# Kernel tuning notes

Hardware: AMD Instinct MI355X
Metric: run time of the kernel (lower is better)

## Reference

```python
import jax, jax.numpy as jnp
import numpy as np

N_NODES = 200000
N_EDGES = 3200000
F_IN = 16
N_CLASSES = 16


def setup_inputs() -> dict:
    key = jax.random.key(0)
    ks = jax.random.split(key, 8)
    s = 1.0 / np.sqrt(F_IN)
    return {
        "x": jax.random.normal(ks[0], (N_NODES, F_IN), dtype=jnp.float32),
        "edge_index": jax.random.randint(ks[1], (2, N_EDGES), 0, N_NODES, dtype=jnp.int32),
        "eps1": jnp.zeros((), dtype=jnp.float32),
        "w1a": jax.random.normal(ks[2], (F_IN, 16), dtype=jnp.float32) * s,
        "b1a": jnp.zeros((16,), dtype=jnp.float32),
        "w1b": jax.random.normal(ks[3], (16, 16), dtype=jnp.float32) * 0.25,
        "b1b": jnp.zeros((16,), dtype=jnp.float32),
        "eps2": jnp.zeros((), dtype=jnp.float32),
        "w2a": jax.random.normal(ks[4], (16, N_CLASSES), dtype=jnp.float32) * 0.25,
        "b2a": jnp.zeros((N_CLASSES,), dtype=jnp.float32),
        "w2b": jax.random.normal(ks[5], (N_CLASSES, N_CLASSES), dtype=jnp.float32) * 0.25,
        "b2b": jnp.zeros((N_CLASSES,), dtype=jnp.float32),
    }


def _gin_conv(x, src, dst, eps, wa, ba, wb, bb, n_nodes):
    # sum aggregation of source-node features into destination nodes
    agg = jax.ops.segment_sum(x[src], dst, num_segments=n_nodes)  # [N, F]
    h = (1.0 + eps) * x + agg
    # 2-layer MLP: Linear -> ReLU -> Linear
    h = jax.nn.relu(h @ wa + ba) @ wb + bb
    return h


def reference(x, edge_index, eps1, w1a, b1a, w1b, b1b, eps2, w2a, b2a, w2b, b2b):
    src, dst = edge_index[0], edge_index[1]
    n = x.shape[0]
    h = jax.nn.relu(_gin_conv(x, src, dst, eps1, w1a, b1a, w1b, b1b, n))
    # F.dropout with training=False is identity (module assumed in eval mode)
    h = _gin_conv(h, src, dst, eps2, w2a, b2a, w2b, b2b, n)
    return jax.nn.log_softmax(h, axis=1)
```

## Files before the change

kernel.cpp:

```cpp
#include <hip/hip_runtime.h>

#define N_NODES 200000
#define N_EDGES 3200000
#define F 16
#define NB 782
#define NB_PAD 832
#define HIST_EPB 8192
#define HIST_BLOCKS ((N_EDGES + HIST_EPB - 1) / HIST_EPB)
#define PART_EPB 8192
#define PART_BLOCKS ((N_EDGES + PART_EPB - 1) / PART_EPB)
#define CAP 5120
#define GIN_T 512


__device__ __forceinline__ unsigned bf16pack2(float lo, float hi) {
    unsigned ul = __float_as_uint(lo);
    unsigned uh = __float_as_uint(hi);
    ul = (ul + 0x7fffu + ((ul >> 16) & 1u)) >> 16;
    uh = (uh + 0x7fffu + ((uh >> 16) & 1u)) >> 16;
    return ul | (uh << 16);
}
#define BLO(w) __uint_as_float((w) << 16)
#define BHI(w) __uint_as_float((w) & 0xffff0000u)

__device__ __forceinline__ void gacc(const unsigned short* __restrict__ xin,
                                     int rec, float acc[16]) {
    const uint4* r = (const uint4*)(xin + (size_t)(rec >> 8) * F);
    uint4 w0 = r[0], w1 = r[1];
    acc[0]  += BLO(w0.x); acc[1]  += BHI(w0.x);
    acc[2]  += BLO(w0.y); acc[3]  += BHI(w0.y);
    acc[4]  += BLO(w0.z); acc[5]  += BHI(w0.z);
    acc[6]  += BLO(w0.w); acc[7]  += BHI(w0.w);
    acc[8]  += BLO(w1.x); acc[9]  += BHI(w1.x);
    acc[10] += BLO(w1.y); acc[11] += BHI(w1.y);
    acc[12] += BLO(w1.z); acc[13] += BHI(w1.z);
    acc[14] += BLO(w1.w); acc[15] += BHI(w1.w);
}


__global__ __launch_bounds__(256) void conv_bf16(const float* __restrict__ x,
                                                 unsigned* __restrict__ xb) {
    int i = blockIdx.x * blockDim.x + threadIdx.x;
    if (i >= N_NODES * F / 8) return;
    const float4* p = (const float4*)(x + (size_t)i * 8);
    float4 a = p[0], b = p[1];
    uint4 r;
    r.x = bf16pack2(a.x, a.y);
    r.y = bf16pack2(a.z, a.w);
    r.z = bf16pack2(b.x, b.y);
    r.w = bf16pack2(b.z, b.w);
    ((uint4*)xb)[i] = r;
}


__global__ __launch_bounds__(256) void bucket_hist(const int* __restrict__ dst,
                                                   int* __restrict__ bcnt) {
    __shared__ int lh[NB];
    const int t = threadIdx.x;
    for (int i = t; i < NB; i += 256) lh[i] = 0;
    __syncthreads();

    const int base4 = blockIdx.x * (HIST_EPB / 4);
    #pragma unroll
    for (int k = 0; k < HIST_EPB / 4 / 256; ++k) {
        int i4 = base4 + k * 256 + t;
        if (i4 < N_EDGES / 4) {
            int4 d = *(const int4*)(dst + i4 * 4);
            atomicAdd(&lh[d.x >> 8], 1);
            atomicAdd(&lh[d.y >> 8], 1);
            atomicAdd(&lh[d.z >> 8], 1);
            atomicAdd(&lh[d.w >> 8], 1);
        }
    }
    __syncthreads();
    for (int i = t; i < NB; i += 256) {
        int v = lh[i];
        if (v) atomicAdd(&bcnt[i], v);
    }
}


__global__ __launch_bounds__(1024) void bucket_scan(const int* __restrict__ bcnt,
                                                    int* __restrict__ bbase,
                                                    int* __restrict__ bcursor) {
    __shared__ int part[1024];
    const int t = threadIdx.x;
    int v = (t < NB) ? bcnt[t] : 0;
    part[t] = v;
    __syncthreads();
    for (int off = 1; off < 1024; off <<= 1) {
        int other = (t >= off) ? part[t - off] : 0;
        __syncthreads();
        part[t] += other;
        __syncthreads();
    }
    if (t < NB) {
        int ex = part[t] - v;
        bbase[t] = ex;
        bcursor[t] = ex;
    }
    if (t == 1023) bbase[NB] = part[1023];
}


__global__ __launch_bounds__(256) void partition_ms(const int* __restrict__ src,
                                                    const int* __restrict__ dst,
                                                    int* __restrict__ bcursor,
                                                    int* __restrict__ ebuf) {
    __shared__ int lh[NB];
    __shared__ int gbase[NB];
    const int t = threadIdx.x;
    for (int i = t; i < NB; i += 256) lh[i] = 0;
    __syncthreads();

    const int base4 = blockIdx.x * (PART_EPB / 4);
    #pragma unroll
    for (int k = 0; k < PART_EPB / 4 / 256; ++k) {
        int i4 = base4 + k * 256 + t;
        if (i4 < N_EDGES / 4) {
            int4 d = *(const int4*)(dst + i4 * 4);
            atomicAdd(&lh[d.x >> 8], 1);
            atomicAdd(&lh[d.y >> 8], 1);
            atomicAdd(&lh[d.z >> 8], 1);
            atomicAdd(&lh[d.w >> 8], 1);
        }
    }
    __syncthreads();
    for (int i = t; i < NB; i += 256) {
        int c = lh[i];
        gbase[i] = c ? atomicAdd(&bcursor[i], c) : 0;
        lh[i] = 0;
    }
    __syncthreads();
    #pragma unroll
    for (int k = 0; k < PART_EPB / 4 / 256; ++k) {
        int i4 = base4 + k * 256 + t;
        if (i4 < N_EDGES / 4) {
            int4 s = *(const int4*)(src + i4 * 4);
            int4 d = *(const int4*)(dst + i4 * 4);
            int b, p;
            b = d.x >> 8; p = atomicAdd(&lh[b], 1); ebuf[gbase[b] + p] = (s.x << 8) | (d.x & 255);
            b = d.y >> 8; p = atomicAdd(&lh[b], 1); ebuf[gbase[b] + p] = (s.y << 8) | (d.y & 255);
            b = d.z >> 8; p = atomicAdd(&lh[b], 1); ebuf[gbase[b] + p] = (s.z << 8) | (d.z & 255);
            b = d.w >> 8; p = atomicAdd(&lh[b], 1); ebuf[gbase[b] + p] = (s.w << 8) | (d.w & 255);
        }
    }
}


template <bool LAYER2>
__global__ __launch_bounds__(GIN_T) void gin_sorted(
    const unsigned short* __restrict__ xin,
    const int* __restrict__ bbase,
    const int* __restrict__ ebuf,
    const float* __restrict__ epsp,
    const float* __restrict__ wa, const float* __restrict__ ba,
    const float* __restrict__ wb, const float* __restrict__ bb,
    void* __restrict__ outp) {
    __shared__ float swa[256], swb[256], sba[16], sbb[16];
    __shared__ int srec[CAP];
    __shared__ int hist[256];
    __shared__ int lofs[256];
    const int t = threadIdx.x;
    const int j = t & 255;
    const int half = t >> 8;
    if (t < 256) { swa[t] = wa[t]; swb[t] = wb[t]; hist[t] = 0; }
    if (t < 16) { sba[t] = ba[t]; sbb[t] = bb[t]; }
    __syncthreads();

    const int b = blockIdx.x;
    const int beg = bbase[b];
    const int end = bbase[b + 1];
    const int sz = end - beg;

    float acc[16];
    #pragma unroll
    for (int q = 0; q < 16; ++q) acc[q] = 0.0f;

    if (sz <= CAP) {
        for (int k = beg + t; k < end; k += GIN_T)
            atomicAdd(&hist[ebuf[k] & 255], 1);
        __syncthreads();
        if (t < 256) lofs[t] = hist[t];
        __syncthreads();
        for (int off = 1; off < 256; off <<= 1) {
            int o = (t >= off && t < 256) ? lofs[t - off] : 0;
            __syncthreads();
            if (t < 256) lofs[t] += o;
            __syncthreads();
        }
        const int myend = lofs[j];
        const int mybeg = myend - hist[j];
        __syncthreads();
        if (t < 256) hist[t] = mybeg;
        __syncthreads();
        for (int k = beg + t; k < end; k += GIN_T) {
            int rec = ebuf[k];
            int p = atomicAdd(&hist[rec & 255], 1);
            srec[p] = rec;
        }
        __syncthreads();
        int k = mybeg + half;
        for (; k + 2 < myend; k += 4) {
            int r0 = srec[k];
            int r1 = srec[k + 2];
            gacc(xin, r0, acc);
            gacc(xin, r1, acc);
        }
        if (k < myend) gacc(xin, srec[k], acc);
    } else {
        if (t < 256) {
            for (int k = beg; k < end; ++k) {
                int rec = ebuf[k];
                if ((rec & 255) == t) gacc(xin, rec, acc);
            }
        }
    }

    __syncthreads();
    float* scratch = (float*)srec;
    if (t >= 256) {
        #pragma unroll
        for (int q = 0; q < 16; ++q) scratch[(t - 256) * 16 + q] = acc[q];
    }
    __syncthreads();
    if (t >= 256) return;

    const int n = b * 256 + t;
    if (n >= N_NODES) return;

    #pragma unroll
    for (int q = 0; q < 16; ++q) acc[q] += scratch[t * 16 + q];

    const float eps = 1.0f + *epsp;
    const uint4* xr = (const uint4*)(xin + (size_t)n * F);
    uint4 w0 = xr[0], w1 = xr[1];
    float h[16];
    h[0]  = fmaf(eps, BLO(w0.x), acc[0]);   h[1]  = fmaf(eps, BHI(w0.x), acc[1]);
    h[2]  = fmaf(eps, BLO(w0.y), acc[2]);   h[3]  = fmaf(eps, BHI(w0.y), acc[3]);
    h[4]  = fmaf(eps, BLO(w0.z), acc[4]);   h[5]  = fmaf(eps, BHI(w0.z), acc[5]);
    h[6]  = fmaf(eps, BLO(w0.w), acc[6]);   h[7]  = fmaf(eps, BHI(w0.w), acc[7]);
    h[8]  = fmaf(eps, BLO(w1.x), acc[8]);   h[9]  = fmaf(eps, BHI(w1.x), acc[9]);
    h[10] = fmaf(eps, BLO(w1.y), acc[10]);  h[11] = fmaf(eps, BHI(w1.y), acc[11]);
    h[12] = fmaf(eps, BLO(w1.z), acc[12]);  h[13] = fmaf(eps, BHI(w1.z), acc[13]);
    h[14] = fmaf(eps, BLO(w1.w), acc[14]);  h[15] = fmaf(eps, BHI(w1.w), acc[15]);

    float m[16];
    #pragma unroll
    for (int jj = 0; jj < 16; ++jj) {
        float a = sba[jj];
        #pragma unroll
        for (int i = 0; i < 16; ++i) a = fmaf(h[i], swa[i * 16 + jj], a);
        m[jj] = fmaxf(a, 0.0f);
    }

    float o[16];
    #pragma unroll
    for (int jj = 0; jj < 16; ++jj) {
        float a = sbb[jj];
        #pragma unroll
        for (int i = 0; i < 16; ++i) a = fmaf(m[i], swb[i * 16 + jj], a);
        o[jj] = LAYER2 ? a : fmaxf(a, 0.0f);
    }

    if (LAYER2) {
        float mx = o[0];
        #pragma unroll
        for (int jj = 1; jj < 16; ++jj) mx = fmaxf(mx, o[jj]);
        float s = 0.0f;
        #pragma unroll
        for (int jj = 0; jj < 16; ++jj) s += expf(o[jj] - mx);
        float lse = mx + logf(s);
        float* orow = (float*)outp + (size_t)n * F;
        #pragma unroll
        for (int q = 0; q < 4; ++q) {
            ((float4*)orow)[q] = make_float4(o[q * 4 + 0] - lse, o[q * 4 + 1] - lse,
                                             o[q * 4 + 2] - lse, o[q * 4 + 3] - lse);
        }
    } else {
        unsigned* orow = (unsigned*)outp + (size_t)n * 8;
        uint4 r0, r1;
        r0.x = bf16pack2(o[0],  o[1]);   r0.y = bf16pack2(o[2],  o[3]);
        r0.z = bf16pack2(o[4],  o[5]);   r0.w = bf16pack2(o[6],  o[7]);
        r1.x = bf16pack2(o[8],  o[9]);   r1.y = bf16pack2(o[10], o[11]);
        r1.z = bf16pack2(o[12], o[13]);  r1.w = bf16pack2(o[14], o[15]);
        ((uint4*)orow)[0] = r0;
        ((uint4*)orow)[1] = r1;
    }
}


__global__ __launch_bounds__(256) void scatter_kernel(
    const float* __restrict__ feat,
    const int* __restrict__ src,
    const int* __restrict__ dst,
    float* __restrict__ agg) {
    int e = blockIdx.x * blockDim.x + threadIdx.x;
    if (e >= N_EDGES) return;
    int s = src[e];
    int d = dst[e];
    const float4* fs = (const float4*)(feat + (size_t)s * F);
    float* ad = agg + (size_t)d * F;
    #pragma unroll
    for (int q = 0; q < 4; ++q) {
        float4 v = fs[q];
        atomicAdd(ad + q * 4 + 0, v.x);
        atomicAdd(ad + q * 4 + 1, v.y);
        atomicAdd(ad + q * 4 + 2, v.z);
        atomicAdd(ad + q * 4 + 3, v.w);
    }
}

template <bool RELU_OUT, bool LOGSOFTMAX>
__global__ __launch_bounds__(256) void mlp_kernel(
    const float* __restrict__ xin,
    const float* __restrict__ agg,
    const float* __restrict__ epsp,
    const float* __restrict__ wa, const float* __restrict__ ba,
    const float* __restrict__ wb, const float* __restrict__ bb,
    float* __restrict__ out) {
    __shared__ float swa[256], swb[256], sba[16], sbb[16];
    int t = threadIdx.x;
    swa[t] = wa[t];
    swb[t] = wb[t];
    if (t < 16) { sba[t] = ba[t]; sbb[t] = bb[t]; }
    __syncthreads();

    int n = blockIdx.x * blockDim.x + t;
    if (n >= N_NODES) return;

    float eps = 1.0f + *epsp;
    const float4* xr = (const float4*)(xin + (size_t)n * F);
    const float4* ar = (const float4*)(agg + (size_t)n * F);
    float h[16];
    #pragma unroll
    for (int q = 0; q < 4; ++q) {
        float4 xv = xr[q];
        float4 av = ar[q];
        h[q * 4 + 0] = fmaf(eps, xv.x, av.x);
        h[q * 4 + 1] = fmaf(eps, xv.y, av.y);
        h[q * 4 + 2] = fmaf(eps, xv.z, av.z);
        h[q * 4 + 3] = fmaf(eps, xv.w, av.w);
    }

    float m[16];
    #pragma unroll
    for (int jj = 0; jj < 16; ++jj) {
        float a = sba[jj];
        #pragma unroll
        for (int i = 0; i < 16; ++i) a = fmaf(h[i], swa[i * 16 + jj], a);
        m[jj] = fmaxf(a, 0.0f);
    }

    float o[16];
    #pragma unroll
    for (int jj = 0; jj < 16; ++jj) {
        float a = sbb[jj];
        #pragma unroll
        for (int i = 0; i < 16; ++i) a = fmaf(m[i], swb[i * 16 + jj], a);
        o[jj] = RELU_OUT ? fmaxf(a, 0.0f) : a;
    }

    if (LOGSOFTMAX) {
        float mx = o[0];
        #pragma unroll
        for (int jj = 1; jj < 16; ++jj) mx = fmaxf(mx, o[jj]);
        float s = 0.0f;
        #pragma unroll
        for (int jj = 0; jj < 16; ++jj) s += expf(o[jj] - mx);
        float lse = mx + logf(s);
        #pragma unroll
        for (int jj = 0; jj < 16; ++jj) o[jj] -= lse;
    }

    float4* orow = (float4*)(out + (size_t)n * F);
    #pragma unroll
    for (int q = 0; q < 4; ++q) {
        orow[q] = make_float4(o[q * 4 + 0], o[q * 4 + 1], o[q * 4 + 2], o[q * 4 + 3]);
    }
}


extern "C" void kernel_launch(void* const* d_in, const int* in_sizes, int n_in,
                              void* d_out, int out_size, void* d_ws, size_t ws_size,
                              hipStream_t stream) {
    const float* x    = (const float*)d_in[0];
    const int*   ei   = (const int*)d_in[1];
    const float* eps1 = (const float*)d_in[2];
    const float* w1a  = (const float*)d_in[3];
    const float* b1a  = (const float*)d_in[4];
    const float* w1b  = (const float*)d_in[5];
    const float* b1b  = (const float*)d_in[6];
    const float* eps2 = (const float*)d_in[7];
    const float* w2a  = (const float*)d_in[8];
    const float* b2a  = (const float*)d_in[9];
    const float* w2b  = (const float*)d_in[10];
    const float* b2b  = (const float*)d_in[11];

    float* out = (float*)d_out;
    const int* src = ei;
    const int* dst = ei + N_EDGES;

    size_t off_bcnt    = 0;
    size_t off_bbase   = off_bcnt + (size_t)NB_PAD * 4;
    size_t off_bcursor = off_bbase + (size_t)NB_PAD * 4;
    size_t off_ebuf    = off_bcursor + (size_t)NB_PAD * 4;
    size_t off_xb      = off_ebuf + (size_t)N_EDGES * 4;
    size_t off_hb      = off_xb + (size_t)N_NODES * F * 2;
    size_t need        = off_hb + (size_t)N_NODES * F * 2;

    if (ws_size >= need) {
        int*            bcnt    = (int*)((char*)d_ws + off_bcnt);
        int*            bbase   = (int*)((char*)d_ws + off_bbase);
        int*            bcursor = (int*)((char*)d_ws + off_bcursor);
        int*            ebuf    = (int*)((char*)d_ws + off_ebuf);
        unsigned short* xb      = (unsigned short*)((char*)d_ws + off_xb);
        unsigned short* hb      = (unsigned short*)((char*)d_ws + off_hb);

        hipMemsetAsync(bcnt, 0, (size_t)NB * 4, stream);
        bucket_hist<<<HIST_BLOCKS, 256, 0, stream>>>(dst, bcnt);
        conv_bf16<<<(N_NODES * F / 8 + 255) / 256, 256, 0, stream>>>(x, (unsigned*)xb);
        bucket_scan<<<1, 1024, 0, stream>>>(bcnt, bbase, bcursor);
        partition_ms<<<PART_BLOCKS, 256, 0, stream>>>(src, dst, bcursor, ebuf);

        gin_sorted<false><<<NB, GIN_T, 0, stream>>>(
            xb, bbase, ebuf, eps1, w1a, b1a, w1b, b1b, hb);
        gin_sorted<true><<<NB, GIN_T, 0, stream>>>(
            hb, bbase, ebuf, eps2, w2a, b2a, w2b, b2b, out);
    } else {
        float* agg = (float*)d_ws;
        const int edge_blocks = (N_EDGES + 255) / 256;
        const int node_blocks = (N_NODES + 255) / 256;
        const size_t agg_bytes = (size_t)N_NODES * F * sizeof(float);

        hipMemsetAsync(agg, 0, agg_bytes, stream);
        scatter_kernel<<<edge_blocks, 256, 0, stream>>>(x, src, dst, agg);
        mlp_kernel<true, false><<<node_blocks, 256, 0, stream>>>(
            x, agg, eps1, w1a, b1a, w1b, b1b, out);

        hipMemsetAsync(agg, 0, agg_bytes, stream);
        scatter_kernel<<<edge_blocks, 256, 0, stream>>>(out, src, dst, agg);
        mlp_kernel<false, true><<<node_blocks, 256, 0, stream>>>(
            out, agg, eps2, w2a, b2a, w2b, b2b, out);
    }
}
```

Baseline: 165.7 us.

## Build full CSR once, then gather per node with 4-lane groups

```diff
diff --git a/kernel.cpp b/kernel.cpp
--- a/kernel.cpp
+++ b/kernel.cpp
@@ -7,10 +7,13 @@
 #define NB_PAD 832
 #define HIST_EPB 8192
 #define HIST_BLOCKS ((N_EDGES + HIST_EPB - 1) / HIST_EPB)
+#define HIST_T 1024
 #define PART_EPB 8192
 #define PART_BLOCKS ((N_EDGES + PART_EPB - 1) / PART_EPB)
+#define PART_T 1024
 #define CAP 5120
-#define GIN_T 512
+#define GIN_NODES 64
+#define GIN_BLOCKS ((N_NODES + GIN_NODES - 1) / GIN_NODES)
 
 
 __device__ __forceinline__ unsigned bf16pack2(float lo, float hi) {
@@ -24,8 +27,8 @@
 #define BHI(w) __uint_as_float((w) & 0xffff0000u)
 
 __device__ __forceinline__ void gacc(const unsigned short* __restrict__ xin,
-                                     int rec, float acc[16]) {
-    const uint4* r = (const uint4*)(xin + (size_t)(rec >> 8) * F);
+                                     int s, float acc[16]) {
+    const uint4* r = (const uint4*)(xin + (size_t)s * F);
     uint4 w0 = r[0], w1 = r[1];
     acc[0]  += BLO(w0.x); acc[1]  += BHI(w0.x);
     acc[2]  += BLO(w0.y); acc[3]  += BHI(w0.y);
@@ -53,17 +56,17 @@
 }
 
 
-__global__ __launch_bounds__(256) void bucket_hist(const int* __restrict__ dst,
-                                                   int* __restrict__ bcnt) {
+__global__ __launch_bounds__(HIST_T) void bucket_hist(const int* __restrict__ dst,
+                                                      int* __restrict__ bcnt) {
     __shared__ int lh[NB];
     const int t = threadIdx.x;
-    for (int i = t; i < NB; i += 256) lh[i] = 0;
+    for (int i = t; i < NB; i += HIST_T) lh[i] = 0;
     __syncthreads();
 
     const int base4 = blockIdx.x * (HIST_EPB / 4);
     #pragma unroll
-    for (int k = 0; k < HIST_EPB / 4 / 256; ++k) {
-        int i4 = base4 + k * 256 + t;
+    for (int k = 0; k < HIST_EPB / 4 / HIST_T; ++k) {
+        int i4 = base4 + k * HIST_T + t;
         if (i4 < N_EDGES / 4) {
             int4 d = *(const int4*)(dst + i4 * 4);
             atomicAdd(&lh[d.x >> 8], 1);
@@ -73,7 +76,7 @@
         }
     }
     __syncthreads();
-    for (int i = t; i < NB; i += 256) {
+    for (int i = t; i < NB; i += HIST_T) {
         int v = lh[i];
         if (v) atomicAdd(&bcnt[i], v);
     }
@@ -103,20 +106,20 @@
 }
 
 
-__global__ __launch_bounds__(256) void partition_ms(const int* __restrict__ src,
-                                                    const int* __restrict__ dst,
-                                                    int* __restrict__ bcursor,
-                                                    int* __restrict__ ebuf) {
+__global__ __launch_bounds__(PART_T) void partition_ms(const int* __restrict__ src,
+                                                       const int* __restrict__ dst,
+                                                       int* __restrict__ bcursor,
+                                                       int* __restrict__ ebuf) {
     __shared__ int lh[NB];
     __shared__ int gbase[NB];
     const int t = threadIdx.x;
-    for (int i = t; i < NB; i += 256) lh[i] = 0;
+    for (int i = t; i < NB; i += PART_T) lh[i] = 0;
     __syncthreads();
 
     const int base4 = blockIdx.x * (PART_EPB / 4);
     #pragma unroll
-    for (int k = 0; k < PART_EPB / 4 / 256; ++k) {
-        int i4 = base4 + k * 256 + t;
+    for (int k = 0; k < PART_EPB / 4 / PART_T; ++k) {
+        int i4 = base4 + k * PART_T + t;
         if (i4 < N_EDGES / 4) {
             int4 d = *(const int4*)(dst + i4 * 4);
             atomicAdd(&lh[d.x >> 8], 1);
@@ -126,15 +129,15 @@
         }
     }
     __syncthreads();
-    for (int i = t; i < NB; i += 256) {
+    for (int i = t; i < NB; i += PART_T) {
         int c = lh[i];
         gbase[i] = c ? atomicAdd(&bcursor[i], c) : 0;
         lh[i] = 0;
     }
     __syncthreads();
     #pragma unroll
-    for (int k = 0; k < PART_EPB / 4 / 256; ++k) {
-        int i4 = base4 + k * 256 + t;
+    for (int k = 0; k < PART_EPB / 4 / PART_T; ++k) {
+        int i4 = base4 + k * PART_T + t;
         if (i4 < N_EDGES / 4) {
             int4 s = *(const int4*)(src + i4 * 4);
             int4 d = *(const int4*)(dst + i4 * 4);
@@ -148,89 +151,106 @@
 }
 
 
+__global__ __launch_bounds__(256) void sort_csr(const int* __restrict__ bbase,
+                                                int* __restrict__ ebuf,
+                                                int* __restrict__ noffs,
+                                                int* __restrict__ scratch) {
+    __shared__ int srec[CAP];
+    __shared__ int hist[256];
+    __shared__ int lofs[256];
+    const int t = threadIdx.x;
+    const int b = blockIdx.x;
+    hist[t] = 0;
+    __syncthreads();
+
+    const int beg = bbase[b];
+    const int end = bbase[b + 1];
+    const int sz = end - beg;
+    const int n = b * 256 + t;
+
+    for (int k = beg + t; k < end; k += 256)
+        atomicAdd(&hist[ebuf[k] & 255], 1);
+    __syncthreads();
+    int v = hist[t];
+    lofs[t] = v;
+    __syncthreads();
+    for (int off = 1; off < 256; off <<= 1) {
+        int o = (t >= off) ? lofs[t - off] : 0;
+        __syncthreads();
+        lofs[t] += o;
+        __syncthreads();
+    }
+    const int myend = lofs[t];
+    const int mybeg = myend - v;
+    __syncthreads();
+    hist[t] = mybeg;
+    __syncthreads();
+
+    if (sz <= CAP) {
+        for (int k = beg + t; k < end; k += 256) {
+            int rec = ebuf[k];
+            int p = atomicAdd(&hist[rec & 255], 1);
+            srec[p] = rec >> 8;
+        }
+        __syncthreads();
+        for (int k = t; k < sz; k += 256) ebuf[beg + k] = srec[k];
+    } else {
+        for (int k = beg + t; k < end; k += 256) scratch[k] = ebuf[k];
+        __syncthreads();
+        for (int k = beg + t; k < end; k += 256) {
+            int rec = scratch[k];
+            int p = atomicAdd(&hist[rec & 255], 1);
+            ebuf[beg + p] = rec >> 8;
+        }
+    }
+
+    if (n < N_NODES) noffs[n] = beg + mybeg;
+    if (b == 0 && t == 0) noffs[N_NODES] = N_EDGES;
+}
+
+
 template <bool LAYER2>
-__global__ __launch_bounds__(GIN_T) void gin_sorted(
+__global__ __launch_bounds__(256) void gin_gather(
     const unsigned short* __restrict__ xin,
-    const int* __restrict__ bbase,
+    const int* __restrict__ noffs,
     const int* __restrict__ ebuf,
     const float* __restrict__ epsp,
     const float* __restrict__ wa, const float* __restrict__ ba,
     const float* __restrict__ wb, const float* __restrict__ bb,
     void* __restrict__ outp) {
     __shared__ float swa[256], swb[256], sba[16], sbb[16];
-    __shared__ int srec[CAP];
-    __shared__ int hist[256];
-    __shared__ int lofs[256];
     const int t = threadIdx.x;
-    const int j = t & 255;
-    const int half = t >> 8;
-    if (t < 256) { swa[t] = wa[t]; swb[t] = wb[t]; hist[t] = 0; }
+    swa[t] = wa[t];
+    swb[t] = wb[t];
     if (t < 16) { sba[t] = ba[t]; sbb[t] = bb[t]; }
     __syncthreads();
 
-    const int b = blockIdx.x;
-    const int beg = bbase[b];
-    const int end = bbase[b + 1];
-    const int sz = end - beg;
+    const int n = blockIdx.x * GIN_NODES + (t >> 2);
+    const int sub = t & 3;
+    if (n >= N_NODES) return;
+
+    const int beg = noffs[n];
+    const int end = noffs[n + 1];
 
     float acc[16];
     #pragma unroll
     for (int q = 0; q < 16; ++q) acc[q] = 0.0f;
 
-    if (sz <= CAP) {
-        for (int k = beg + t; k < end; k += GIN_T)
-            atomicAdd(&hist[ebuf[k] & 255], 1);
-        __syncthreads();
-        if (t < 256) lofs[t] = hist[t];
-        __syncthreads();
-        for (int off = 1; off < 256; off <<= 1) {
-            int o = (t >= off && t < 256) ? lofs[t - off] : 0;
-            __syncthreads();
-            if (t < 256) lofs[t] += o;
-            __syncthreads();
-        }
-        const int myend = lofs[j];
-        const int mybeg = myend - hist[j];
-        __syncthreads();
-        if (t < 256) hist[t] = mybeg;
-        __syncthreads();
-        for (int k = beg + t; k < end; k += GIN_T) {
-            int rec = ebuf[k];
-            int p = atomicAdd(&hist[rec & 255], 1);
-            srec[p] = rec;
-        }
-        __syncthreads();
-        int k = mybeg + half;
-        for (; k + 2 < myend; k += 4) {
-            int r0 = srec[k];
-            int r1 = srec[k + 2];
-            gacc(xin, r0, acc);
-            gacc(xin, r1, acc);
-        }
-        if (k < myend) gacc(xin, srec[k], acc);
-    } else {
-        if (t < 256) {
-            for (int k = beg; k < end; ++k) {
-                int rec = ebuf[k];
-                if ((rec & 255) == t) gacc(xin, rec, acc);
-            }
-        }
-    }
-
-    __syncthreads();
-    float* scratch = (float*)srec;
-    if (t >= 256) {
-        #pragma unroll
-        for (int q = 0; q < 16; ++q) scratch[(t - 256) * 16 + q] = acc[q];
-    }
-    __syncthreads();
-    if (t >= 256) return;
-
-    const int n = b * 256 + t;
-    if (n >= N_NODES) return;
-
-    #pragma unroll
-    for (int q = 0; q < 16; ++q) acc[q] += scratch[t * 16 + q];
+    int k = beg + sub;
+    for (; k + 4 < end; k += 8) {
+        int s0 = ebuf[k];
+        int s1 = ebuf[k + 4];
+        gacc(xin, s0, acc);
+        gacc(xin, s1, acc);
+    }
+    if (k < end) gacc(xin, ebuf[k], acc);
+
+    #pragma unroll
+    for (int q = 0; q < 16; ++q) {
+        acc[q] += __shfl_xor(acc[q], 1);
+        acc[q] += __shfl_xor(acc[q], 2);
+    }
+    if (sub != 0) return;
 
     const float eps = 1.0f + *epsp;
     const uint4* xr = (const uint4*)(xin + (size_t)n * F);
@@ -404,7 +424,8 @@
     size_t off_bcnt    = 0;
     size_t off_bbase   = off_bcnt + (size_t)NB_PAD * 4;
     size_t off_bcursor = off_bbase + (size_t)NB_PAD * 4;
-    size_t off_ebuf    = off_bcursor + (size_t)NB_PAD * 4;
+    size_t off_noffs   = off_bcursor + (size_t)NB_PAD * 4;
+    size_t off_ebuf    = off_noffs + ((size_t)N_NODES + 64) * 4;
     size_t off_xb      = off_ebuf + (size_t)N_EDGES * 4;
     size_t off_hb      = off_xb + (size_t)N_NODES * F * 2;
     size_t need        = off_hb + (size_t)N_NODES * F * 2;
@@ -413,20 +434,22 @@
         int*            bcnt    = (int*)((char*)d_ws + off_bcnt);
         int*            bbase   = (int*)((char*)d_ws + off_bbase);
         int*            bcursor = (int*)((char*)d_ws + off_bcursor);
+        int*            noffs   = (int*)((char*)d_ws + off_noffs);
         int*            ebuf    = (int*)((char*)d_ws + off_ebuf);
         unsigned short* xb      = (unsigned short*)((char*)d_ws + off_xb);
         unsigned short* hb      = (unsigned short*)((char*)d_ws + off_hb);
 
         hipMemsetAsync(bcnt, 0, (size_t)NB * 4, stream);
-        bucket_hist<<<HIST_BLOCKS, 256, 0, stream>>>(dst, bcnt);
+        bucket_hist<<<HIST_BLOCKS, HIST_T, 0, stream>>>(dst, bcnt);
         conv_bf16<<<(N_NODES * F / 8 + 255) / 256, 256, 0, stream>>>(x, (unsigned*)xb);
         bucket_scan<<<1, 1024, 0, stream>>>(bcnt, bbase, bcursor);
-        partition_ms<<<PART_BLOCKS, 256, 0, stream>>>(src, dst, bcursor, ebuf);
-
-        gin_sorted<false><<<NB, GIN_T, 0, stream>>>(
-            xb, bbase, ebuf, eps1, w1a, b1a, w1b, b1b, hb);
-        gin_sorted<true><<<NB, GIN_T, 0, stream>>>(
-            hb, bbase, ebuf, eps2, w2a, b2a, w2b, b2b, out);
+        partition_ms<<<PART_BLOCKS, PART_T, 0, stream>>>(src, dst, bcursor, ebuf);
+        sort_csr<<<NB, 256, 0, stream>>>(bbase, ebuf, noffs, (int*)d_out);
+
+        gin_gather<false><<<GIN_BLOCKS, 256, 0, stream>>>(
+            xb, noffs, ebuf, eps1, w1a, b1a, w1b, b1b, hb);
+        gin_gather<true><<<GIN_BLOCKS, 256, 0, stream>>>(
+            hb, noffs, ebuf, eps2, w2a, b2a, w2b, b2b, out);
     } else {
         float* agg = (float*)d_ws;
         const int edge_blocks = (N_EDGES + 255) / 256;
```

Result: faster. 159.3 us (-3.9%).
